# Performance work log

Hardware: AMD Instinct MI355X
Metric: run time of the kernel (lower is better)

## Reference

```python
import jax, jax.numpy as jnp
import numpy as np

B, D, H, V, L, T = 64, 512, 1024, 32000, 2, 32  # batch, word_dim, hidden, vocab, layers, steps


def setup_inputs() -> dict:
    key = jax.random.key(0)
    ks = jax.random.split(key, 8)
    s = lambda k, shp: jax.random.normal(k, shp, dtype=jnp.float32) * 0.02
    return {
        "features": jax.random.normal(ks[0], (B, D), dtype=jnp.float32),
        "embed": s(ks[1], (V, D)),
        "Wih0": s(ks[2], (4 * H, D)), "Whh0": s(ks[3], (4 * H, H)),
        "bih0": jnp.zeros((4 * H,), jnp.float32), "bhh0": jnp.zeros((4 * H,), jnp.float32),
        "Wih1": s(ks[4], (4 * H, H)), "Whh1": s(ks[5], (4 * H, H)),
        "bih1": jnp.zeros((4 * H,), jnp.float32), "bhh1": jnp.zeros((4 * H,), jnp.float32),
        "Wout": s(ks[6], (V, H)), "bout": jnp.zeros((V,), jnp.float32),
    }


def _lstm_cell(x, h, c, Wih, Whh, bih, bhh):
    # torch gate order: input, forget, cell, output
    g = x @ Wih.T + h @ Whh.T + bih + bhh
    i, f, gg, o = jnp.split(g, 4, axis=-1)
    c2 = jax.nn.sigmoid(f) * c + jax.nn.sigmoid(i) * jnp.tanh(gg)
    h2 = jax.nn.sigmoid(o) * jnp.tanh(c2)
    return h2, c2


def reference(features, embed, Wih0, Whh0, bih0, bhh0, Wih1, Whh1, bih1, bhh1, Wout, bout):
    layers = [(Wih0, Whh0, bih0, bhh0), (Wih1, Whh1, bih1, bhh1)]
    h0 = jnp.zeros((L, B, H), jnp.float32)
    c0 = jnp.zeros((L, B, H), jnp.float32)

    def step(carry, _):
        x, h, c = carry  # x: [B, D] current input token embedding (or features at t=0)
        hs, cs = [], []
        inp = x
        for l, (Wih, Whh, bih, bhh) in enumerate(layers):
            hn, cn = _lstm_cell(inp, h[l], c[l], Wih, Whh, bih, bhh)
            hs.append(hn); cs.append(cn)
            inp = hn
        logits = inp @ Wout.T + bout          # [B, V]
        pred = jnp.argmax(logits, axis=-1)    # greedy token
        xn = embed[pred]                      # [B, D]
        return (xn, jnp.stack(hs), jnp.stack(cs)), pred

    _, ids = jax.lax.scan(step, (features, h0, c0), None, length=T)  # ids: [T, B]
    return ids.T.astype(jnp.int32)  # sampled_ids: [B, T]
```

## Files before the change

### kernel.cpp

```cpp
#include <hip/hip_runtime.h>
#include <math.h>

#define BB 64
#define DD 512
#define HH 1024
#define VV 32000
#define NG 4096
#define TT 32
#define KS 8
#define VBLK 500

typedef __bf16 bf16x8 __attribute__((ext_vector_type(8)));
typedef float  f32x4  __attribute__((ext_vector_type(4)));

__device__ __forceinline__ void split_bf16(float x, unsigned short* hi, unsigned short* lo)
{
    unsigned u = __float_as_uint(x);
    unsigned r = (u + 0x7fffu + ((u >> 16) & 1u)) & 0xffff0000u;
    *hi = (unsigned short)(r >> 16);
    float rem = x - __uint_as_float(r);
    unsigned u2 = __float_as_uint(rem);
    unsigned r2 = u2 + 0x7fffu + ((u2 >> 16) & 1u);
    *lo = (unsigned short)(r2 >> 16);
}

__global__ __launch_bounds__(256)
void split_k(const float* __restrict__ src, unsigned short* __restrict__ hi,
             unsigned short* __restrict__ lo, int n4)
{
    const int stride = gridDim.x * 256;
    for (int i = blockIdx.x * 256 + threadIdx.x; i < n4; i += stride) {
        const float4 v = ((const float4*)src)[i];
        ushort4 h, l;
        split_bf16(v.x, &h.x, &l.x);
        split_bf16(v.y, &h.y, &l.y);
        split_bf16(v.z, &h.z, &l.z);
        split_bf16(v.w, &h.w, &l.w);
        ((ushort4*)hi)[i] = h;
        ((ushort4*)lo)[i] = l;
    }
}

__global__ __launch_bounds__(256)
void gates_mfma_k(const unsigned short* __restrict__ Xhi, const unsigned short* __restrict__ Xlo,
                  const int K0,
                  const unsigned short* __restrict__ Hhi, const unsigned short* __restrict__ Hlo,
                  const unsigned short* __restrict__ Wihhi, const unsigned short* __restrict__ Wihlo,
                  const unsigned short* __restrict__ Whhhi, const unsigned short* __restrict__ Whhlo,
                  float* __restrict__ P)
{
    __shared__ unsigned short Ah[64][72], Al[64][72], Wh[64][72], Wl[64][72];

    const int j0   = blockIdx.x * 64;
    const int y    = blockIdx.y;
    const int tid  = threadIdx.x;
    const int wv   = tid >> 6;
    const int lane = tid & 63;
    const int l15  = lane & 15;
    const int q    = lane >> 4;
    const int sr   = tid >> 3;
    const int sc   = tid & 7;

    f32x4 acc[4] = {{0,0,0,0},{0,0,0,0},{0,0,0,0},{0,0,0,0}};

#pragma unroll
    for (int seg = 0; seg < 2; seg++) {
        const unsigned short* __restrict__ Ahi = seg ? Hhi : Xhi;
        const unsigned short* __restrict__ Alo = seg ? Hlo : Xlo;
        const unsigned short* __restrict__ Whi = seg ? Whhhi : Wihhi;
        const unsigned short* __restrict__ Wlo = seg ? Whhlo : Wihlo;
        const int K  = seg ? HH : K0;
        const int kc = K >> 3;
        const int kend = y * kc + kc;

        for (int kb = y * kc; kb < kend; kb += 64) {
#pragma unroll
            for (int qq = 0; qq < 2; qq++) {
                const int row = sr + 32 * qq;
                *(uint4*)&Ah[row][sc * 8] = *(const uint4*)(Ahi + (size_t)row * K + kb + sc * 8);
                *(uint4*)&Al[row][sc * 8] = *(const uint4*)(Alo + (size_t)row * K + kb + sc * 8);
                *(uint4*)&Wh[row][sc * 8] = *(const uint4*)(Whi + (size_t)(j0 + row) * K + kb + sc * 8);
                *(uint4*)&Wl[row][sc * 8] = *(const uint4*)(Wlo + (size_t)(j0 + row) * K + kb + sc * 8);
            }
            __syncthreads();
#pragma unroll
            for (int ks = 0; ks < 2; ks++) {
                const int ko = ks * 32 + q * 8;
                const bf16x8 ah = *(const bf16x8*)&Ah[16 * wv + l15][ko];
                const bf16x8 al = *(const bf16x8*)&Al[16 * wv + l15][ko];
#pragma unroll
                for (int t = 0; t < 4; t++) {
                    const bf16x8 bh = *(const bf16x8*)&Wh[16 * t + l15][ko];
                    const bf16x8 bl = *(const bf16x8*)&Wl[16 * t + l15][ko];
                    acc[t] = __builtin_amdgcn_mfma_f32_16x16x32_bf16(ah, bl, acc[t], 0, 0, 0);
                    acc[t] = __builtin_amdgcn_mfma_f32_16x16x32_bf16(al, bh, acc[t], 0, 0, 0);
                    acc[t] = __builtin_amdgcn_mfma_f32_16x16x32_bf16(ah, bh, acc[t], 0, 0, 0);
                }
            }
            __syncthreads();
        }
    }

    float* __restrict__ Pout = P + (size_t)y * (BB * NG);
#pragma unroll
    for (int reg = 0; reg < 4; reg++) {
        const int row = 16 * wv + q * 4 + reg;
#pragma unroll
        for (int t = 0; t < 4; t++)
            Pout[(size_t)row * NG + j0 + 16 * t + l15] = acc[t][reg];
    }
}

__global__ __launch_bounds__(256)
void cell_k(const float* __restrict__ P, const float* __restrict__ bih,
            const float* __restrict__ bhh, float* __restrict__ c,
            unsigned short* __restrict__ hhi, unsigned short* __restrict__ hlo)
{
    const int tid = blockIdx.x * 256 + threadIdx.x;
    const int b = tid >> 10;
    const int u = tid & (HH - 1);

    float gi = bih[u]          + bhh[u];
    float gf = bih[HH + u]     + bhh[HH + u];
    float gg = bih[2 * HH + u] + bhh[2 * HH + u];
    float go = bih[3 * HH + u] + bhh[3 * HH + u];

#pragma unroll
    for (int s = 0; s < KS; s++) {
        const float* ps = P + (size_t)s * (BB * NG) + (size_t)b * NG;
        gi += ps[u];
        gf += ps[HH + u];
        gg += ps[2 * HH + u];
        go += ps[3 * HH + u];
    }

    const float si = 1.0f / (1.0f + expf(-gi));
    const float sf = 1.0f / (1.0f + expf(-gf));
    const float so = 1.0f / (1.0f + expf(-go));
    const float cn = sf * c[tid] + si * tanhf(gg);
    const float hn = so * tanhf(cn);
    c[tid] = cn;
    split_bf16(hn, &hhi[tid], &hlo[tid]);
}

__global__ __launch_bounds__(256)
void logits_mfma_k(const unsigned short* __restrict__ Ahi,
                   const unsigned short* __restrict__ Alo,
                   const unsigned short* __restrict__ Whi,
                   const unsigned short* __restrict__ Wlo,
                   const float* __restrict__ bout,
                   float* __restrict__ pv, int* __restrict__ pi)
{
    __shared__ unsigned short Ah[64][72], Al[64][72], Wh[64][72], Wl[64][72];
    __shared__ float rv[64][16];
    __shared__ int   ri[64][16];

    const int v0   = blockIdx.x * 64;
    const int tid  = threadIdx.x;
    const int wv   = tid >> 6;
    const int lane = tid & 63;
    const int l15  = lane & 15;
    const int q    = lane >> 4;
    const int sr   = tid >> 3;
    const int sc   = tid & 7;

    f32x4 acc[4] = {{0,0,0,0},{0,0,0,0},{0,0,0,0},{0,0,0,0}};

    for (int kb = 0; kb < HH; kb += 64) {
#pragma unroll
        for (int qq = 0; qq < 2; qq++) {
            const int row = sr + 32 * qq;
            *(uint4*)&Ah[row][sc * 8] = *(const uint4*)(Ahi + (size_t)row * HH + kb + sc * 8);
            *(uint4*)&Al[row][sc * 8] = *(const uint4*)(Alo + (size_t)row * HH + kb + sc * 8);
            *(uint4*)&Wh[row][sc * 8] = *(const uint4*)(Whi + (size_t)(v0 + row) * HH + kb + sc * 8);
            *(uint4*)&Wl[row][sc * 8] = *(const uint4*)(Wlo + (size_t)(v0 + row) * HH + kb + sc * 8);
        }
        __syncthreads();

#pragma unroll
        for (int ks = 0; ks < 2; ks++) {
            const int ko = ks * 32 + q * 8;
            const bf16x8 ah = *(const bf16x8*)&Ah[16 * wv + l15][ko];
            const bf16x8 al = *(const bf16x8*)&Al[16 * wv + l15][ko];
#pragma unroll
            for (int t = 0; t < 4; t++) {
                const bf16x8 bh = *(const bf16x8*)&Wh[16 * t + l15][ko];
                const bf16x8 bl = *(const bf16x8*)&Wl[16 * t + l15][ko];
                acc[t] = __builtin_amdgcn_mfma_f32_16x16x32_bf16(ah, bl, acc[t], 0, 0, 0);
                acc[t] = __builtin_amdgcn_mfma_f32_16x16x32_bf16(al, bh, acc[t], 0, 0, 0);
                acc[t] = __builtin_amdgcn_mfma_f32_16x16x32_bf16(ah, bh, acc[t], 0, 0, 0);
            }
        }
        __syncthreads();
    }

#pragma unroll
    for (int reg = 0; reg < 4; reg++) {
        float best = -INFINITY;
        int bid = 0x7fffffff;
#pragma unroll
        for (int t = 0; t < 4; t++) {
            const int id = v0 + 16 * t + l15;
            const float v = acc[t][reg] + bout[id];
            if (v > best || (v == best && id < bid)) { best = v; bid = id; }
        }
        rv[16 * wv + q * 4 + reg][l15] = best;
        ri[16 * wv + q * 4 + reg][l15] = bid;
    }
    __syncthreads();

    if (tid < 64) {
        float best = -INFINITY;
        int bid = 0x7fffffff;
        for (int k = 0; k < 16; k++) {
            const float v = rv[tid][k];
            const int id = ri[tid][k];
            if (v > best || (v == best && id < bid)) { best = v; bid = id; }
        }
        pv[(size_t)tid * VBLK + blockIdx.x] = best;
        pi[(size_t)tid * VBLK + blockIdx.x] = bid;
    }
}

__global__ __launch_bounds__(256)
void final_k(const float* __restrict__ pv, const int* __restrict__ pi,
             const float* __restrict__ embed, unsigned short* __restrict__ xhi,
             unsigned short* __restrict__ xlo, int* __restrict__ out, int t)
{
    __shared__ float sv[256];
    __shared__ int   si[256];
    const int b = blockIdx.x;
    const int tid = threadIdx.x;

    float best = -INFINITY;
    int bid = 0x7fffffff;
    for (int k = tid; k < VBLK; k += 256) {
        float v = pv[(size_t)b * VBLK + k];
        int id = pi[(size_t)b * VBLK + k];
        if (v > best || (v == best && id < bid)) { best = v; bid = id; }
    }
    sv[tid] = best; si[tid] = bid;
    __syncthreads();
    for (int s = 128; s > 0; s >>= 1) {
        if (tid < s) {
            float v = sv[tid + s]; int id = si[tid + s];
            if (v > sv[tid] || (v == sv[tid] && id < si[tid])) { sv[tid] = v; si[tid] = id; }
        }
        __syncthreads();
    }
    const int pred = si[0];
    if (tid == 0) out[(size_t)b * TT + t] = pred;
    for (int d = tid; d < DD; d += 256) {
        const float v = embed[(size_t)pred * DD + d];
        split_bf16(v, &xhi[(size_t)b * DD + d], &xlo[(size_t)b * DD + d]);
    }
}

extern "C" void kernel_launch(void* const* d_in, const int* in_sizes, int n_in,
                              void* d_out, int out_size, void* d_ws, size_t ws_size,
                              hipStream_t stream)
{
    const float* features = (const float*)d_in[0];
    const float* embed    = (const float*)d_in[1];
    const float* Wih0     = (const float*)d_in[2];
    const float* Whh0     = (const float*)d_in[3];
    const float* bih0     = (const float*)d_in[4];
    const float* bhh0     = (const float*)d_in[5];
    const float* Wih1     = (const float*)d_in[6];
    const float* Whh1     = (const float*)d_in[7];
    const float* bih1     = (const float*)d_in[8];
    const float* bhh1     = (const float*)d_in[9];
    const float* Wout     = (const float*)d_in[10];
    const float* bout     = (const float*)d_in[11];
    int* out = (int*)d_out;

    float* ws = (float*)d_ws;
    float* c0 = ws;
    float* c1 = c0 + BB * HH;
    unsigned short* hhi0 = (unsigned short*)(c1 + BB * HH);
    unsigned short* hlo0 = hhi0 + BB * HH;
    unsigned short* hhi1 = hlo0 + BB * HH;
    unsigned short* hlo1 = hhi1 + BB * HH;
    unsigned short* xhi  = hlo1 + BB * HH;
    unsigned short* xlo  = xhi + BB * DD;
    float* part = (float*)(xlo + BB * DD);
    float* pv   = part + (size_t)KS * BB * NG;
    int*   pi   = (int*)(pv + BB * VBLK);
    unsigned short* wih0h = (unsigned short*)(pi + BB * VBLK);
    unsigned short* wih0l = wih0h + (size_t)NG * DD;
    unsigned short* whh0h = wih0l + (size_t)NG * DD;
    unsigned short* whh0l = whh0h + (size_t)NG * HH;
    unsigned short* wih1h = whh0l + (size_t)NG * HH;
    unsigned short* wih1l = wih1h + (size_t)NG * HH;
    unsigned short* whh1h = wih1l + (size_t)NG * HH;
    unsigned short* whh1l = whh1h + (size_t)NG * HH;
    unsigned short* wouth = whh1l + (size_t)NG * HH;
    unsigned short* woutl = wouth + (size_t)VV * HH;

    hipMemsetAsync(c0, 0, (size_t)2 * BB * HH * sizeof(float)
                        + (size_t)4 * BB * HH * sizeof(unsigned short), stream);

    const dim3 blk(256);
    const dim3 ggates(NG / 64, KS);
    const dim3 gcell(BB * HH / 256);
    const dim3 glog(VBLK);
    const dim3 gfin(BB);

    {
        auto gs = [](int n4) { int g = (n4 + 255) / 256; return dim3(g > 2048 ? 2048 : g); };
        split_k<<<gs(NG * DD / 4), blk, 0, stream>>>(Wih0, wih0h, wih0l, NG * DD / 4);
        split_k<<<gs(NG * HH / 4), blk, 0, stream>>>(Whh0, whh0h, whh0l, NG * HH / 4);
        split_k<<<gs(NG * HH / 4), blk, 0, stream>>>(Wih1, wih1h, wih1l, NG * HH / 4);
        split_k<<<gs(NG * HH / 4), blk, 0, stream>>>(Whh1, whh1h, whh1l, NG * HH / 4);
        split_k<<<gs(VV * HH / 4), blk, 0, stream>>>(Wout, wouth, woutl, VV * HH / 4);
        split_k<<<gs(BB * DD / 4), blk, 0, stream>>>(features, xhi, xlo, BB * DD / 4);
    }

    for (int t = 0; t < TT; t++) {
        gates_mfma_k<<<ggates, blk, 0, stream>>>(xhi, xlo, DD, hhi0, hlo0,
                                                 wih0h, wih0l, whh0h, whh0l, part);
        cell_k<<<gcell, blk, 0, stream>>>(part, bih0, bhh0, c0, hhi0, hlo0);
        gates_mfma_k<<<ggates, blk, 0, stream>>>(hhi0, hlo0, HH, hhi1, hlo1,
                                                 wih1h, wih1l, whh1h, whh1l, part);
        cell_k<<<gcell, blk, 0, stream>>>(part, bih1, bhh1, c1, hhi1, hlo1);
        logits_mfma_k<<<glog, blk, 0, stream>>>(hhi1, hlo1, wouth, woutl, bout, pv, pi);
        final_k<<<gfin, blk, 0, stream>>>(pv, pi, embed, xhi, xlo, out, t);
    }
}
```

Measured before the change: 2.243 ms.

## Fuse LSTM cell into gate GEMM and argmax into logits via last-block reduction

```diff
diff --git a/kernel.cpp b/kernel.cpp
--- a/kernel.cpp
+++ b/kernel.cpp
@@ -42,14 +42,47 @@
 }
 
 __global__ __launch_bounds__(256)
-void gates_mfma_k(const unsigned short* __restrict__ Xhi, const unsigned short* __restrict__ Xlo,
-                  const int K0,
-                  const unsigned short* __restrict__ Hhi, const unsigned short* __restrict__ Hlo,
-                  const unsigned short* __restrict__ Wihhi, const unsigned short* __restrict__ Wihlo,
-                  const unsigned short* __restrict__ Whhhi, const unsigned short* __restrict__ Whhlo,
-                  float* __restrict__ P)
+void split_gate_k(const float* __restrict__ src, unsigned short* __restrict__ hi,
+                  unsigned short* __restrict__ lo, int kshift, int n4)
+{
+    const int stride = gridDim.x * 256;
+    const int K4m = (1 << kshift) - 1;
+    for (int i = blockIdx.x * 256 + threadIdx.x; i < n4; i += stride) {
+        const int r = i >> kshift;
+        const int k4 = i & K4m;
+        const int u = r >> 2, g = r & 3;
+        const float4 v = ((const float4*)src)[((size_t)(g * HH + u) << kshift) + k4];
+        ushort4 h, l;
+        split_bf16(v.x, &h.x, &l.x);
+        split_bf16(v.y, &h.y, &l.y);
+        split_bf16(v.z, &h.z, &l.z);
+        split_bf16(v.w, &h.w, &l.w);
+        ((ushort4*)hi)[i] = h;
+        ((ushort4*)lo)[i] = l;
+    }
+}
+
+__global__ __launch_bounds__(256)
+void bias_k(const float* __restrict__ bih, const float* __restrict__ bhh,
+            float* __restrict__ bsum)
+{
+    const int r = blockIdx.x * 256 + threadIdx.x;
+    const int u = r >> 2, g = r & 3;
+    bsum[r] = bih[g * HH + u] + bhh[g * HH + u];
+}
+
+__global__ __launch_bounds__(256)
+void gatescell_k(const unsigned short* __restrict__ Ahi0, const unsigned short* __restrict__ Alo0,
+                 const int K0,
+                 const unsigned short* __restrict__ Ahi1, const unsigned short* __restrict__ Alo1,
+                 const unsigned short* __restrict__ Wihi, const unsigned short* __restrict__ Wilo,
+                 const unsigned short* __restrict__ Whhi, const unsigned short* __restrict__ Whlo,
+                 const float* __restrict__ bsum, float* __restrict__ c,
+                 unsigned short* __restrict__ Hhi, unsigned short* __restrict__ Hlo,
+                 float* __restrict__ P, int* __restrict__ cnt)
 {
     __shared__ unsigned short Ah[64][72], Al[64][72], Wh[64][72], Wl[64][72];
+    __shared__ int s_last;
 
     const int j0   = blockIdx.x * 64;
     const int y    = blockIdx.y;
@@ -65,10 +98,10 @@
 
 #pragma unroll
     for (int seg = 0; seg < 2; seg++) {
-        const unsigned short* __restrict__ Ahi = seg ? Hhi : Xhi;
-        const unsigned short* __restrict__ Alo = seg ? Hlo : Xlo;
-        const unsigned short* __restrict__ Whi = seg ? Whhhi : Wihhi;
-        const unsigned short* __restrict__ Wlo = seg ? Whhlo : Wihlo;
+        const unsigned short* __restrict__ Ahi = seg ? Ahi1 : Ahi0;
+        const unsigned short* __restrict__ Alo = seg ? Alo1 : Alo0;
+        const unsigned short* __restrict__ Whi = seg ? Whhi : Wihi;
+        const unsigned short* __restrict__ Wlo = seg ? Whlo : Wilo;
         const int K  = seg ? HH : K0;
         const int kc = K >> 3;
         const int kend = y * kc + kc;
@@ -109,51 +142,58 @@
         for (int t = 0; t < 4; t++)
             Pout[(size_t)row * NG + j0 + 16 * t + l15] = acc[t][reg];
     }
-}
-
-__global__ __launch_bounds__(256)
-void cell_k(const float* __restrict__ P, const float* __restrict__ bih,
-            const float* __restrict__ bhh, float* __restrict__ c,
-            unsigned short* __restrict__ hhi, unsigned short* __restrict__ hlo)
-{
-    const int tid = blockIdx.x * 256 + threadIdx.x;
-    const int b = tid >> 10;
-    const int u = tid & (HH - 1);
-
-    float gi = bih[u]          + bhh[u];
-    float gf = bih[HH + u]     + bhh[HH + u];
-    float gg = bih[2 * HH + u] + bhh[2 * HH + u];
-    float go = bih[3 * HH + u] + bhh[3 * HH + u];
-
-#pragma unroll
-    for (int s = 0; s < KS; s++) {
-        const float* ps = P + (size_t)s * (BB * NG) + (size_t)b * NG;
-        gi += ps[u];
-        gf += ps[HH + u];
-        gg += ps[2 * HH + u];
-        go += ps[3 * HH + u];
-    }
-
-    const float si = 1.0f / (1.0f + expf(-gi));
-    const float sf = 1.0f / (1.0f + expf(-gf));
-    const float so = 1.0f / (1.0f + expf(-go));
-    const float cn = sf * c[tid] + si * tanhf(gg);
-    const float hn = so * tanhf(cn);
-    c[tid] = cn;
-    split_bf16(hn, &hhi[tid], &hlo[tid]);
-}
-
-__global__ __launch_bounds__(256)
-void logits_mfma_k(const unsigned short* __restrict__ Ahi,
+
+    __syncthreads();
+    if (tid == 0) {
+        const int prev = __hip_atomic_fetch_add(cnt + blockIdx.x, 1,
+                                                __ATOMIC_ACQ_REL, __HIP_MEMORY_SCOPE_AGENT);
+        s_last = (prev == KS - 1);
+    }
+    __syncthreads();
+    if (!s_last) return;
+    if (tid == 0)
+        __hip_atomic_store(cnt + blockIdx.x, 0, __ATOMIC_RELAXED, __HIP_MEMORY_SCOPE_AGENT);
+
+    const int u0 = blockIdx.x * 16;
+#pragma unroll
+    for (int p = 0; p < 4; p++) {
+        const int idx = tid + 256 * p;
+        const int b = idx >> 4;
+        const int u = u0 + (idx & 15);
+        float4 g = *(const float4*)&bsum[4 * u];
+#pragma unroll
+        for (int s = 0; s < KS; s++) {
+            const float4 p4 = *(const float4*)&P[(size_t)s * (BB * NG) + (size_t)b * NG + 4 * u];
+            g.x += p4.x; g.y += p4.y; g.z += p4.z; g.w += p4.w;
+        }
+        const float si = 1.0f / (1.0f + expf(-g.x));
+        const float sf = 1.0f / (1.0f + expf(-g.y));
+        const float so = 1.0f / (1.0f + expf(-g.w));
+        const float cn = sf * c[b * HH + u] + si * tanhf(g.z);
+        const float hn = so * tanhf(cn);
+        c[b * HH + u] = cn;
+        split_bf16(hn, &Hhi[b * HH + u], &Hlo[b * HH + u]);
+    }
+}
+
+__global__ __launch_bounds__(256)
+void logitsfinal_k(const unsigned short* __restrict__ Ahi,
                    const unsigned short* __restrict__ Alo,
                    const unsigned short* __restrict__ Whi,
                    const unsigned short* __restrict__ Wlo,
                    const float* __restrict__ bout,
-                   float* __restrict__ pv, int* __restrict__ pi)
+                   float* __restrict__ pv, int* __restrict__ pi,
+                   const float* __restrict__ embed,
+                   unsigned short* __restrict__ xhi, unsigned short* __restrict__ xlo,
+                   int* __restrict__ out, const int t, int* __restrict__ cnt)
 {
     __shared__ unsigned short Ah[64][72], Al[64][72], Wh[64][72], Wl[64][72];
     __shared__ float rv[64][16];
     __shared__ int   ri[64][16];
+    __shared__ float fv[256];
+    __shared__ int   fi[256];
+    __shared__ int   s_tok[64];
+    __shared__ int   s_last;
 
     const int v0   = blockIdx.x * 64;
     const int tid  = threadIdx.x;
@@ -183,12 +223,12 @@
             const bf16x8 ah = *(const bf16x8*)&Ah[16 * wv + l15][ko];
             const bf16x8 al = *(const bf16x8*)&Al[16 * wv + l15][ko];
 #pragma unroll
-            for (int t = 0; t < 4; t++) {
-                const bf16x8 bh = *(const bf16x8*)&Wh[16 * t + l15][ko];
-                const bf16x8 bl = *(const bf16x8*)&Wl[16 * t + l15][ko];
-                acc[t] = __builtin_amdgcn_mfma_f32_16x16x32_bf16(ah, bl, acc[t], 0, 0, 0);
-                acc[t] = __builtin_amdgcn_mfma_f32_16x16x32_bf16(al, bh, acc[t], 0, 0, 0);
-                acc[t] = __builtin_amdgcn_mfma_f32_16x16x32_bf16(ah, bh, acc[t], 0, 0, 0);
+            for (int tt = 0; tt < 4; tt++) {
+                const bf16x8 bh = *(const bf16x8*)&Wh[16 * tt + l15][ko];
+                const bf16x8 bl = *(const bf16x8*)&Wl[16 * tt + l15][ko];
+                acc[tt] = __builtin_amdgcn_mfma_f32_16x16x32_bf16(ah, bl, acc[tt], 0, 0, 0);
+                acc[tt] = __builtin_amdgcn_mfma_f32_16x16x32_bf16(al, bh, acc[tt], 0, 0, 0);
+                acc[tt] = __builtin_amdgcn_mfma_f32_16x16x32_bf16(ah, bh, acc[tt], 0, 0, 0);
             }
         }
         __syncthreads();
@@ -199,9 +239,9 @@
         float best = -INFINITY;
         int bid = 0x7fffffff;
 #pragma unroll
-        for (int t = 0; t < 4; t++) {
-            const int id = v0 + 16 * t + l15;
-            const float v = acc[t][reg] + bout[id];
+        for (int tt = 0; tt < 4; tt++) {
+            const int id = v0 + 16 * tt + l15;
+            const float v = acc[tt][reg] + bout[id];
             if (v > best || (v == best && id < bid)) { best = v; bid = id; }
         }
         rv[16 * wv + q * 4 + reg][l15] = best;
@@ -220,39 +260,53 @@
         pv[(size_t)tid * VBLK + blockIdx.x] = best;
         pi[(size_t)tid * VBLK + blockIdx.x] = bid;
     }
-}
-
-__global__ __launch_bounds__(256)
-void final_k(const float* __restrict__ pv, const int* __restrict__ pi,
-             const float* __restrict__ embed, unsigned short* __restrict__ xhi,
-             unsigned short* __restrict__ xlo, int* __restrict__ out, int t)
-{
-    __shared__ float sv[256];
-    __shared__ int   si[256];
-    const int b = blockIdx.x;
-    const int tid = threadIdx.x;
-
-    float best = -INFINITY;
-    int bid = 0x7fffffff;
-    for (int k = tid; k < VBLK; k += 256) {
-        float v = pv[(size_t)b * VBLK + k];
-        int id = pi[(size_t)b * VBLK + k];
-        if (v > best || (v == best && id < bid)) { best = v; bid = id; }
-    }
-    sv[tid] = best; si[tid] = bid;
-    __syncthreads();
-    for (int s = 128; s > 0; s >>= 1) {
-        if (tid < s) {
-            float v = sv[tid + s]; int id = si[tid + s];
-            if (v > sv[tid] || (v == sv[tid] && id < si[tid])) { sv[tid] = v; si[tid] = id; }
-        }
-        __syncthreads();
-    }
-    const int pred = si[0];
-    if (tid == 0) out[(size_t)b * TT + t] = pred;
-    for (int d = tid; d < DD; d += 256) {
-        const float v = embed[(size_t)pred * DD + d];
-        split_bf16(v, &xhi[(size_t)b * DD + d], &xlo[(size_t)b * DD + d]);
+
+    __syncthreads();
+    if (tid == 0) {
+        const int prev = __hip_atomic_fetch_add(cnt, 1,
+                                                __ATOMIC_ACQ_REL, __HIP_MEMORY_SCOPE_AGENT);
+        s_last = (prev == (int)gridDim.x - 1);
+    }
+    __syncthreads();
+    if (!s_last) return;
+    if (tid == 0)
+        __hip_atomic_store(cnt, 0, __ATOMIC_RELAXED, __HIP_MEMORY_SCOPE_AGENT);
+
+    {
+        const int row = tid >> 2, pt = tid & 3;
+        float best = -INFINITY;
+        int bid = 0x7fffffff;
+        for (int k = pt; k < VBLK; k += 4) {
+            const float v = pv[(size_t)row * VBLK + k];
+            const int id = pi[(size_t)row * VBLK + k];
+            if (v > best || (v == best && id < bid)) { best = v; bid = id; }
+        }
+        fv[tid] = best; fi[tid] = bid;
+    }
+    __syncthreads();
+    if ((tid & 3) == 0) {
+        const int row = tid >> 2;
+        float best = fv[tid]; int bid = fi[tid];
+#pragma unroll
+        for (int j = 1; j < 4; j++) {
+            const float v = fv[tid + j]; const int id = fi[tid + j];
+            if (v > best || (v == best && id < bid)) { best = v; bid = id; }
+        }
+        out[(size_t)row * TT + t] = bid;
+        s_tok[row] = bid;
+    }
+    __syncthreads();
+
+    for (int i = tid; i < BB * (DD / 4); i += 256) {
+        const int b = i >> 7, d4 = i & 127;
+        const float4 e = ((const float4*)(embed + (size_t)s_tok[b] * DD))[d4];
+        ushort4 h4, l4;
+        split_bf16(e.x, &h4.x, &l4.x);
+        split_bf16(e.y, &h4.y, &l4.y);
+        split_bf16(e.z, &h4.z, &l4.z);
+        split_bf16(e.w, &h4.w, &l4.w);
+        *(ushort4*)&xhi[(size_t)b * DD + d4 * 4] = h4;
+        *(ushort4*)&xlo[(size_t)b * DD + d4 * 4] = l4;
     }
 }
 
@@ -274,19 +328,21 @@
     const float* bout     = (const float*)d_in[11];
     int* out = (int*)d_out;
 
+    const size_t BH = (size_t)BB * HH;
+
     float* ws = (float*)d_ws;
     float* c0 = ws;
-    float* c1 = c0 + BB * HH;
-    unsigned short* hhi0 = (unsigned short*)(c1 + BB * HH);
-    unsigned short* hlo0 = hhi0 + BB * HH;
-    unsigned short* hhi1 = hlo0 + BB * HH;
-    unsigned short* hlo1 = hhi1 + BB * HH;
-    unsigned short* xhi  = hlo1 + BB * HH;
-    unsigned short* xlo  = xhi + BB * DD;
-    float* part = (float*)(xlo + BB * DD);
+    float* c1 = c0 + BH;
+    unsigned short* hbuf = (unsigned short*)(c1 + BH);
+    unsigned short* xhi  = hbuf + 8 * BH;
+    unsigned short* xlo  = xhi + (size_t)BB * DD;
+    int* cnt = (int*)(xlo + (size_t)BB * DD);
+    float* part = (float*)((char*)cnt + 1024);
     float* pv   = part + (size_t)KS * BB * NG;
-    int*   pi   = (int*)(pv + BB * VBLK);
-    unsigned short* wih0h = (unsigned short*)(pi + BB * VBLK);
+    int*   pi   = (int*)(pv + (size_t)BB * VBLK);
+    float* bsum0 = (float*)(pi + (size_t)BB * VBLK);
+    float* bsum1 = bsum0 + NG;
+    unsigned short* wih0h = (unsigned short*)(bsum1 + NG);
     unsigned short* wih0l = wih0h + (size_t)NG * DD;
     unsigned short* whh0h = wih0l + (size_t)NG * DD;
     unsigned short* whh0l = whh0h + (size_t)NG * HH;
@@ -297,33 +353,42 @@
     unsigned short* wouth = whh1l + (size_t)NG * HH;
     unsigned short* woutl = wouth + (size_t)VV * HH;
 
-    hipMemsetAsync(c0, 0, (size_t)2 * BB * HH * sizeof(float)
-                        + (size_t)4 * BB * HH * sizeof(unsigned short), stream);
+    const size_t zlen = 2 * BH * sizeof(float) + 8 * BH * sizeof(unsigned short)
+                      + 2 * (size_t)BB * DD * sizeof(unsigned short) + 1024;
+    hipMemsetAsync(c0, 0, zlen, stream);
 
     const dim3 blk(256);
     const dim3 ggates(NG / 64, KS);
-    const dim3 gcell(BB * HH / 256);
     const dim3 glog(VBLK);
-    const dim3 gfin(BB);
 
     {
         auto gs = [](int n4) { int g = (n4 + 255) / 256; return dim3(g > 2048 ? 2048 : g); };
-        split_k<<<gs(NG * DD / 4), blk, 0, stream>>>(Wih0, wih0h, wih0l, NG * DD / 4);
-        split_k<<<gs(NG * HH / 4), blk, 0, stream>>>(Whh0, whh0h, whh0l, NG * HH / 4);
-        split_k<<<gs(NG * HH / 4), blk, 0, stream>>>(Wih1, wih1h, wih1l, NG * HH / 4);
-        split_k<<<gs(NG * HH / 4), blk, 0, stream>>>(Whh1, whh1h, whh1l, NG * HH / 4);
+        split_gate_k<<<gs(NG * DD / 4), blk, 0, stream>>>(Wih0, wih0h, wih0l, 7, NG * DD / 4);
+        split_gate_k<<<gs(NG * HH / 4), blk, 0, stream>>>(Whh0, whh0h, whh0l, 8, NG * HH / 4);
+        split_gate_k<<<gs(NG * HH / 4), blk, 0, stream>>>(Wih1, wih1h, wih1l, 8, NG * HH / 4);
+        split_gate_k<<<gs(NG * HH / 4), blk, 0, stream>>>(Whh1, whh1h, whh1l, 8, NG * HH / 4);
         split_k<<<gs(VV * HH / 4), blk, 0, stream>>>(Wout, wouth, woutl, VV * HH / 4);
         split_k<<<gs(BB * DD / 4), blk, 0, stream>>>(features, xhi, xlo, BB * DD / 4);
-    }
+        bias_k<<<dim3(NG / 256), blk, 0, stream>>>(bih0, bhh0, bsum0);
+        bias_k<<<dim3(NG / 256), blk, 0, stream>>>(bih1, bhh1, bsum1);
+    }
+
+    auto hp = [&](int l, int p, int comp) {
+        return hbuf + (((size_t)(l * 2 + p)) * 2 + comp) * BH;
+    };
 
     for (int t = 0; t < TT; t++) {
-        gates_mfma_k<<<ggates, blk, 0, stream>>>(xhi, xlo, DD, hhi0, hlo0,
-                                                 wih0h, wih0l, whh0h, whh0l, part);
-        cell_k<<<gcell, blk, 0, stream>>>(part, bih0, bhh0, c0, hhi0, hlo0);
-        gates_mfma_k<<<ggates, blk, 0, stream>>>(hhi0, hlo0, HH, hhi1, hlo1,
-                                                 wih1h, wih1l, whh1h, whh1l, part);
-        cell_k<<<gcell, blk, 0, stream>>>(part, bih1, bhh1, c1, hhi1, hlo1);
-        logits_mfma_k<<<glog, blk, 0, stream>>>(hhi1, hlo1, wouth, woutl, bout, pv, pi);
-        final_k<<<gfin, blk, 0, stream>>>(pv, pi, embed, xhi, xlo, out, t);
-    }
-}
+        const int pp = t & 1;
+        gatescell_k<<<ggates, blk, 0, stream>>>(
+            xhi, xlo, DD, hp(0, pp, 0), hp(0, pp, 1),
+            wih0h, wih0l, whh0h, whh0l, bsum0, c0,
+            hp(0, pp ^ 1, 0), hp(0, pp ^ 1, 1), part, cnt);
+        gatescell_k<<<ggates, blk, 0, stream>>>(
+            hp(0, pp ^ 1, 0), hp(0, pp ^ 1, 1), HH, hp(1, pp, 0), hp(1, pp, 1),
+            wih1h, wih1l, whh1h, whh1l, bsum1, c1,
+            hp(1, pp ^ 1, 0), hp(1, pp ^ 1, 1), part, cnt + 64);
+        logitsfinal_k<<<glog, blk, 0, stream>>>(
+            hp(1, pp ^ 1, 0), hp(1, pp ^ 1, 1), wouth, woutl, bout,
+            pv, pi, embed, xhi, xlo, out, t, cnt + 128);
+    }
+}
```

New measurement: 5.962 ms. 2.66x slower.
